# Kernel optimization log

Measured on AMD Instinct MI355X. Metric: run time of the kernel, lower is better.

The kernel has to match this reference:

```python
import jax, jax.numpy as jnp
import numpy as np

N, E, C_IN, H, K = 16384, 524288, 128, 64, 64


def setup_inputs() -> dict:
    key = jax.random.key(0)
    ks = jax.random.split(key, 6)
    x = jax.random.normal(ks[0], (N, C_IN), dtype=jnp.float32)
    edge_index = jax.random.randint(ks[1], (2, E), 0, N, dtype=jnp.int32)
    edge_weight = jax.random.uniform(ks[2], (E,), dtype=jnp.float32)
    sc = lambda f: 1.0 / np.sqrt(f)
    # GCNConv lin (no bias inside lin; separate bias), Glorot-ish init
    W1 = jax.random.normal(ks[3], (C_IN, H), dtype=jnp.float32) * sc(C_IN)
    b1 = jnp.zeros((H,), jnp.float32)
    # DMoNPooling MLP: Linear(H,H) then Linear(H,K), no activation between (act=None)
    Wm1 = jax.random.normal(ks[4], (H, H), dtype=jnp.float32) * sc(H)
    bm1 = jnp.zeros((H,), jnp.float32)
    Wm2 = jax.random.normal(ks[5], (H, K), dtype=jnp.float32) * sc(H)
    bm2 = jnp.zeros((K,), jnp.float32)
    return dict(x=x, edge_index=edge_index, edge_weight=edge_weight,
                W1=W1, b1=b1, Wm1=Wm1, bm1=bm1, Wm2=Wm2, bm2=bm2)


def gcn_conv(x, edge_index, edge_weight, W, b, n):
    # GCNConv: add self-loops (weight 1), symmetric deg^-1/2 normalization,
    # aggregate messages from source (row) into target (col).
    row, col = edge_index[0], edge_index[1]
    loop = jnp.arange(n, dtype=edge_index.dtype)
    row = jnp.concatenate([row, loop])
    col = jnp.concatenate([col, loop])
    w = jnp.concatenate([edge_weight, jnp.ones((n,), edge_weight.dtype)])
    deg = jax.ops.segment_sum(w, col, num_segments=n)
    dis = jnp.where(deg > 0, jax.lax.rsqrt(deg), 0.0)
    norm = dis[row] * w * dis[col]
    xw = x @ W  # [N, H]
    out = jax.ops.segment_sum(xw[row] * norm[:, None], col, num_segments=n)
    return out + b


def dmon_pool(h, adj, Wm1, bm1, Wm2, bm2):
    # eval mode: dropout disabled
    s = jax.nn.softmax((h @ Wm1 + bm1) @ Wm2 + bm2, axis=-1)  # [N, K]
    k = s.shape[-1]
    out_adj = s.T @ (adj @ s)  # [K, K]

    # Spectral (modularity) loss; degrees = einsum('ijk->ik', adj) = column sums
    deg = adj.sum(axis=0)  # [N]
    m = deg.sum() / 2
    ca = s.T @ deg  # [K], equals degrees^T s as well (symmetric roles)
    normalizer = jnp.outer(ca, ca) / 2 / m
    spectral_loss = -jnp.trace(out_adj - normalizer) / 2 / m

    # Orthogonality loss
    ss = s.T @ s  # [K, K]
    ss_fro = jnp.sqrt(jnp.sum(ss * ss))
    i_fro = jnp.sqrt(jnp.float32(k))  # ||I_K||_F
    diff = ss / ss_fro - jnp.eye(k, dtype=ss.dtype) / i_fro
    ortho_loss = jnp.sqrt(jnp.sum(diff * diff))

    # Cluster size loss
    cluster_size = s.sum(axis=0)  # [K]
    cluster_loss = jnp.sqrt(jnp.sum(cluster_size * cluster_size)) / h.shape[0] * i_fro - 1.0

    return s, spectral_loss, ortho_loss, cluster_loss


def reference(x, edge_index, edge_weight, W1, b1, Wm1, bm1, Wm2, bm2):
    h = jax.nn.relu(gcn_conv(x, edge_index, edge_weight, W1, b1, N))
    # to_dense_adj(edge_index): dense [N, N], duplicate edges summed
    adj = jnp.zeros((N, N), h.dtype).at[edge_index[0], edge_index[1]].add(1.0)
    s, spec, ortho, clus = dmon_pool(h, adj, Wm1, bm1, Wm2, bm2)
    return s[None], spec + ortho + clus
```

## Files before the change

### kernel.cpp

```cpp
#include <hip/hip_runtime.h>
#include <hip/hip_bf16.h>

typedef float          f4  __attribute__((ext_vector_type(4)));
typedef unsigned short us4 __attribute__((ext_vector_type(4)));
typedef int            i2  __attribute__((ext_vector_type(2)));

template <typename T>
__device__ __forceinline__ T ntload(const T* p) { return __builtin_nontemporal_load(p); }

__device__ __forceinline__ unsigned short f2bf(float f) {
    unsigned u = __float_as_uint(f);
    return (unsigned short)((u + 0x7FFF + ((u >> 16) & 1)) >> 16);
}
__device__ __forceinline__ float bf2f(unsigned short h) {
    return __uint_as_float((unsigned)h << 16);
}

__global__ __launch_bounds__(256) void k_degxw(const int* __restrict__ ei,
                      const float* __restrict__ ew,
                      unsigned long long* __restrict__ deg_rep,
                      const float* __restrict__ x, const float* __restrict__ W1,
                      float* __restrict__ xw, unsigned short* __restrict__ xw16,
                      int N, int E) {
    __shared__ float w1l[128 * 64];
    __shared__ f4    xt[16][32];
    if (blockIdx.x < 2048) {
        int e = blockIdx.x * 256 + threadIdx.x;
        if (e < E) {
            int c = ntload(ei + E + e);
            float w = ntload(ew + e);
            unsigned q = (unsigned)__float2uint_rn(w * 16777216.f);
            unsigned long long p = (1ULL << 40) | (unsigned long long)q;
            atomicAdd(&deg_rep[(size_t)(blockIdx.x & 7) * N + c], p);
        }
        return;
    }
    int xbid = blockIdx.x - 2048;
    for (int t = threadIdx.x; t < 128 * 64; t += 256) w1l[t] = W1[t];
    int lane = threadIdx.x & 63;
    int wv   = threadIdx.x >> 6;
    for (int base = xbid * 16; base < N; base += 512 * 16) {
        __syncthreads();
        for (int t = threadIdx.x; t < 16 * 32; t += 256)
            ((f4*)xt)[t] = ntload((const f4*)x + (size_t)base * 32 + t);
        __syncthreads();
        int r0 = wv * 4;
        float a0 = 0.f, a1 = 0.f, a2 = 0.f, a3 = 0.f;
#pragma unroll
        for (int q = 0; q < 32; ++q) {
            f4 x0 = xt[r0][q], x1 = xt[r0 + 1][q], x2 = xt[r0 + 2][q], x3 = xt[r0 + 3][q];
            float wa = w1l[(4 * q + 0) * 64 + lane];
            float wb = w1l[(4 * q + 1) * 64 + lane];
            float wc = w1l[(4 * q + 2) * 64 + lane];
            float wd = w1l[(4 * q + 3) * 64 + lane];
            a0 = fmaf(x0.x, wa, a0); a0 = fmaf(x0.y, wb, a0); a0 = fmaf(x0.z, wc, a0); a0 = fmaf(x0.w, wd, a0);
            a1 = fmaf(x1.x, wa, a1); a1 = fmaf(x1.y, wb, a1); a1 = fmaf(x1.z, wc, a1); a1 = fmaf(x1.w, wd, a1);
            a2 = fmaf(x2.x, wa, a2); a2 = fmaf(x2.y, wb, a2); a2 = fmaf(x2.z, wc, a2); a2 = fmaf(x2.w, wd, a2);
            a3 = fmaf(x3.x, wa, a3); a3 = fmaf(x3.y, wb, a3); a3 = fmaf(x3.z, wc, a3); a3 = fmaf(x3.w, wd, a3);
        }
        int gr = base + r0;
        __builtin_nontemporal_store(a0, xw + (size_t)(gr + 0) * 64 + lane);
        __builtin_nontemporal_store(a1, xw + (size_t)(gr + 1) * 64 + lane);
        __builtin_nontemporal_store(a2, xw + (size_t)(gr + 2) * 64 + lane);
        __builtin_nontemporal_store(a3, xw + (size_t)(gr + 3) * 64 + lane);
        xw16[(size_t)(gr + 0) * 64 + lane] = f2bf(a0);
        xw16[(size_t)(gr + 1) * 64 + lane] = f2bf(a1);
        xw16[(size_t)(gr + 2) * 64 + lane] = f2bf(a2);
        xw16[(size_t)(gr + 3) * 64 + lane] = f2bf(a3);
    }
}

__global__ void k_red(const unsigned long long* __restrict__ deg_rep,
                      int* __restrict__ off_rep, int* __restrict__ cnt,
                      float* __restrict__ dis, int N) {
    int c = blockIdx.x * blockDim.x + threadIdx.x;
    if (c >= N) return;
    int run = 0;
    unsigned long long wsum = 0;
#pragma unroll
    for (int rep = 0; rep < 8; ++rep) {
        unsigned long long p = deg_rep[(size_t)rep * N + c];
        off_rep[(size_t)rep * N + c] = run;
        run += (int)(p >> 40);
        wsum += (p & ((1ULL << 40) - 1));
    }
    cnt[c] = run;
    dis[c] = rsqrtf((float)wsum * (1.f / 16777216.f) + 1.0f);
}

__global__ void k_scan(const int* __restrict__ cnt, int* __restrict__ offs, int N) {
    __shared__ int part[1024];
    int tid = threadIdx.x;
    int C = (N + 1023) / 1024;
    int base = tid * C;
    int loc[16];
    int sum = 0;
#pragma unroll
    for (int i = 0; i < 16; ++i) {
        if (i < C) {
            int idx = base + i;
            loc[i] = sum;
            sum += (idx < N) ? cnt[idx] : 0;
        }
    }
    part[tid] = sum;
    __syncthreads();
    for (int o = 1; o < 1024; o <<= 1) {
        int t = (tid >= o) ? part[tid - o] : 0;
        __syncthreads();
        part[tid] += t;
        __syncthreads();
    }
    int excl = part[tid] - sum;
#pragma unroll
    for (int i = 0; i < 16; ++i) {
        if (i < C) {
            int idx = base + i;
            if (idx < N) offs[idx] = excl + loc[i];
        }
    }
    if (tid == 1023) offs[N] = part[tid];
}

__global__ void k_bucket(const int* __restrict__ ei, const float* __restrict__ ew,
                         const float* __restrict__ dis, const int* __restrict__ offs,
                         const int* __restrict__ off_rep, int* __restrict__ cursor_rep,
                         i2* __restrict__ barr, int N, int E) {
    int e = blockIdx.x * blockDim.x + threadIdx.x;
    if (e < E) {
        int rep = blockIdx.x & 7;
        int r = ntload(ei + e), c = ntload(ei + E + e);
        float norm = dis[r] * ntload(ew + e) * dis[c];
        size_t rc = (size_t)rep * N + c;
        int pos = offs[c] + off_rep[rc] + atomicAdd(&cursor_rep[rc], 1);
        i2 rec; rec.x = r; rec.y = __float_as_int(norm);
        __builtin_nontemporal_store(rec, barr + pos);
    }
}

__global__ __launch_bounds__(256) void k_gather(const int* __restrict__ offs,
                         const i2* __restrict__ barr,
                         const float* __restrict__ xw, const unsigned short* __restrict__ xw16,
                         const float* __restrict__ dis,
                         const float* __restrict__ b1, float* __restrict__ h, int N) {
    int lane = threadIdx.x & 63;
    int sub = lane >> 4, q = lane & 15;
    int wid  = blockIdx.x * 4 + (threadIdx.x >> 6);
    int nw   = 4 * gridDim.x;
    const us4* xw16v = (const us4*)xw16;
    for (int cp = wid; cp < (N >> 1); cp += nw) {
        int c0 = 2 * cp, c1 = c0 + 1;
        int beg = ntload(offs + c0), mid = ntload(offs + c1), end = ntload(offs + c1 + 1);
        f4 A0 = {0.f, 0.f, 0.f, 0.f}, A1 = A0, B0 = A0, B1 = A0;
        for (int i = beg; i < end; i += 64) {
            int nloc = min(64, end - i);
            bool ok = (i + lane < end);
            i2 b = ok ? ntload(barr + i + lane) : (i2){0, 0};
            int   rv = b.x;
            float nv = __int_as_float(b.y);
            int jmax = (nloc + 3) >> 2;
            int j = 0;
            for (; j + 4 <= jmax; j += 4) {
                int e0 = 4 * j + sub;
                int g0 = i + e0;
                int   r0 = __shfl(rv, e0),      r1 = __shfl(rv, e0 + 4);
                int   r2 = __shfl(rv, e0 + 8),  r3 = __shfl(rv, e0 + 12);
                float n0 = __shfl(nv, e0),      n1 = __shfl(nv, e0 + 4);
                float n2 = __shfl(nv, e0 + 8),  n3 = __shfl(nv, e0 + 12);
                us4 u0 = xw16v[(size_t)r0 * 16 + q];
                us4 u1 = xw16v[(size_t)r1 * 16 + q];
                us4 u2 = xw16v[(size_t)r2 * 16 + q];
                us4 u3 = xw16v[(size_t)r3 * 16 + q];
                float a0w = (g0      < mid) ? n0 : 0.f, b0w = n0 - a0w;
                float a1w = (g0 + 4  < mid) ? n1 : 0.f, b1w = n1 - a1w;
                float a2w = (g0 + 8  < mid) ? n2 : 0.f, b2w = n2 - a2w;
                float a3w = (g0 + 12 < mid) ? n3 : 0.f, b3w = n3 - a3w;
                A0.x = fmaf(bf2f(u0.x), a0w, A0.x); A0.y = fmaf(bf2f(u0.y), a0w, A0.y);
                A0.z = fmaf(bf2f(u0.z), a0w, A0.z); A0.w = fmaf(bf2f(u0.w), a0w, A0.w);
                B0.x = fmaf(bf2f(u0.x), b0w, B0.x); B0.y = fmaf(bf2f(u0.y), b0w, B0.y);
                B0.z = fmaf(bf2f(u0.z), b0w, B0.z); B0.w = fmaf(bf2f(u0.w), b0w, B0.w);
                A1.x = fmaf(bf2f(u1.x), a1w, A1.x); A1.y = fmaf(bf2f(u1.y), a1w, A1.y);
                A1.z = fmaf(bf2f(u1.z), a1w, A1.z); A1.w = fmaf(bf2f(u1.w), a1w, A1.w);
                B1.x = fmaf(bf2f(u1.x), b1w, B1.x); B1.y = fmaf(bf2f(u1.y), b1w, B1.y);
                B1.z = fmaf(bf2f(u1.z), b1w, B1.z); B1.w = fmaf(bf2f(u1.w), b1w, B1.w);
                A0.x = fmaf(bf2f(u2.x), a2w, A0.x); A0.y = fmaf(bf2f(u2.y), a2w, A0.y);
                A0.z = fmaf(bf2f(u2.z), a2w, A0.z); A0.w = fmaf(bf2f(u2.w), a2w, A0.w);
                B0.x = fmaf(bf2f(u2.x), b2w, B0.x); B0.y = fmaf(bf2f(u2.y), b2w, B0.y);
                B0.z = fmaf(bf2f(u2.z), b2w, B0.z); B0.w = fmaf(bf2f(u2.w), b2w, B0.w);
                A1.x = fmaf(bf2f(u3.x), a3w, A1.x); A1.y = fmaf(bf2f(u3.y), a3w, A1.y);
                A1.z = fmaf(bf2f(u3.z), a3w, A1.z); A1.w = fmaf(bf2f(u3.w), a3w, A1.w);
                B1.x = fmaf(bf2f(u3.x), b3w, B1.x); B1.y = fmaf(bf2f(u3.y), b3w, B1.y);
                B1.z = fmaf(bf2f(u3.z), b3w, B1.z); B1.w = fmaf(bf2f(u3.w), b3w, B1.w);
            }
            for (; j < jmax; ++j) {
                int e = 4 * j + sub;
                int g = i + e;
                int   r  = __shfl(rv, e);
                float nm = __shfl(nv, e);
                us4 u = xw16v[(size_t)r * 16 + q];
                float aw = (g < mid) ? nm : 0.f, bw = nm - aw;
                A0.x = fmaf(bf2f(u.x), aw, A0.x); A0.y = fmaf(bf2f(u.y), aw, A0.y);
                A0.z = fmaf(bf2f(u.z), aw, A0.z); A0.w = fmaf(bf2f(u.w), aw, A0.w);
                B0.x = fmaf(bf2f(u.x), bw, B0.x); B0.y = fmaf(bf2f(u.y), bw, B0.y);
                B0.z = fmaf(bf2f(u.z), bw, B0.z); B0.w = fmaf(bf2f(u.w), bw, B0.w);
            }
        }
        A0.x += A1.x; A0.y += A1.y; A0.z += A1.z; A0.w += A1.w;
        B0.x += B1.x; B0.y += B1.y; B0.z += B1.z; B0.w += B1.w;
        A0.x += __shfl_xor(A0.x, 16); A0.y += __shfl_xor(A0.y, 16);
        A0.z += __shfl_xor(A0.z, 16); A0.w += __shfl_xor(A0.w, 16);
        B0.x += __shfl_xor(B0.x, 16); B0.y += __shfl_xor(B0.y, 16);
        B0.z += __shfl_xor(B0.z, 16); B0.w += __shfl_xor(B0.w, 16);
        A0.x += __shfl_xor(A0.x, 32); A0.y += __shfl_xor(A0.y, 32);
        A0.z += __shfl_xor(A0.z, 32); A0.w += __shfl_xor(A0.w, 32);
        B0.x += __shfl_xor(B0.x, 32); B0.y += __shfl_xor(B0.y, 32);
        B0.z += __shfl_xor(B0.z, 32); B0.w += __shfl_xor(B0.w, 32);
        f4 bb = ((const f4*)b1)[q];
        f4 self0 = ntload((const f4*)xw + (size_t)c0 * 16 + q);
        f4 self1 = ntload((const f4*)xw + (size_t)c1 * 16 + q);
        float d0 = dis[c0], d1 = dis[c1];
        float dd0 = d0 * d0, dd1 = d1 * d1;
        f4 v0, v1;
        v0.x = A0.x + self0.x * dd0 + bb.x; v0.y = A0.y + self0.y * dd0 + bb.y;
        v0.z = A0.z + self0.z * dd0 + bb.z; v0.w = A0.w + self0.w * dd0 + bb.w;
        v1.x = B0.x + self1.x * dd1 + bb.x; v1.y = B0.y + self1.y * dd1 + bb.y;
        v1.z = B0.z + self1.z * dd1 + bb.z; v1.w = B0.w + self1.w * dd1 + bb.w;
        v0.x = v0.x > 0.f ? v0.x : 0.f; v0.y = v0.y > 0.f ? v0.y : 0.f;
        v0.z = v0.z > 0.f ? v0.z : 0.f; v0.w = v0.w > 0.f ? v0.w : 0.f;
        v1.x = v1.x > 0.f ? v1.x : 0.f; v1.y = v1.y > 0.f ? v1.y : 0.f;
        v1.z = v1.z > 0.f ? v1.z : 0.f; v1.w = v1.w > 0.f ? v1.w : 0.f;
        if (sub == 0) {
            __builtin_nontemporal_store(v0, (f4*)h + (size_t)c0 * 16 + q);
            __builtin_nontemporal_store(v1, (f4*)h + (size_t)c1 * 16 + q);
        }
    }
}

__global__ __launch_bounds__(256) void k_mlp(const float* __restrict__ h,
                      const float* __restrict__ Wm1, const float* __restrict__ bm1,
                      const float* __restrict__ Wm2, const float* __restrict__ bm2,
                      float* __restrict__ s, unsigned short* __restrict__ s16, int N) {
    __shared__ float w1l[4096], w2l[4096], b1l[64], b2l[64];
    __shared__ f4    ht[16][16];
    __shared__ float tt[4][4][64];
    for (int t = threadIdx.x; t < 4096; t += 256) {
        w1l[t] = Wm1[t];
        w2l[t] = Wm2[t];
    }
    if (threadIdx.x < 64) {
        b1l[threadIdx.x] = bm1[threadIdx.x];
        b2l[threadIdx.x] = bm2[threadIdx.x];
    }
    int lane = threadIdx.x & 63;
    int wv   = threadIdx.x >> 6;
    for (int base = blockIdx.x * 16; base < N; base += gridDim.x * 16) {
        __syncthreads();
        for (int t = threadIdx.x; t < 16 * 16; t += 256)
            ((f4*)ht)[t] = ntload((const f4*)h + (size_t)base * 16 + t);
        __syncthreads();
        int r0 = wv * 4;
        float t0 = b1l[lane], t1 = t0, t2 = t0, t3 = t0;
#pragma unroll
        for (int q = 0; q < 16; ++q) {
            f4 h0 = ht[r0][q], h1 = ht[r0 + 1][q], h2 = ht[r0 + 2][q], h3 = ht[r0 + 3][q];
            float wa = w1l[(4 * q + 0) * 64 + lane];
            float wb = w1l[(4 * q + 1) * 64 + lane];
            float wc = w1l[(4 * q + 2) * 64 + lane];
            float wd = w1l[(4 * q + 3) * 64 + lane];
            t0 = fmaf(h0.x, wa, t0); t0 = fmaf(h0.y, wb, t0); t0 = fmaf(h0.z, wc, t0); t0 = fmaf(h0.w, wd, t0);
            t1 = fmaf(h1.x, wa, t1); t1 = fmaf(h1.y, wb, t1); t1 = fmaf(h1.z, wc, t1); t1 = fmaf(h1.w, wd, t1);
            t2 = fmaf(h2.x, wa, t2); t2 = fmaf(h2.y, wb, t2); t2 = fmaf(h2.z, wc, t2); t2 = fmaf(h2.w, wd, t2);
            t3 = fmaf(h3.x, wa, t3); t3 = fmaf(h3.y, wb, t3); t3 = fmaf(h3.z, wc, t3); t3 = fmaf(h3.w, wd, t3);
        }
        tt[wv][0][lane] = t0; tt[wv][1][lane] = t1;
        tt[wv][2][lane] = t2; tt[wv][3][lane] = t3;
        __syncthreads();
        float g0 = b2l[lane], g1 = g0, g2 = g0, g3 = g0;
#pragma unroll
        for (int q = 0; q < 16; ++q) {
            f4 u0 = ((f4*)tt[wv][0])[q], u1 = ((f4*)tt[wv][1])[q];
            f4 u2 = ((f4*)tt[wv][2])[q], u3 = ((f4*)tt[wv][3])[q];
            float wa = w2l[(4 * q + 0) * 64 + lane];
            float wb = w2l[(4 * q + 1) * 64 + lane];
            float wc = w2l[(4 * q + 2) * 64 + lane];
            float wd = w2l[(4 * q + 3) * 64 + lane];
            g0 = fmaf(u0.x, wa, g0); g0 = fmaf(u0.y, wb, g0); g0 = fmaf(u0.z, wc, g0); g0 = fmaf(u0.w, wd, g0);
            g1 = fmaf(u1.x, wa, g1); g1 = fmaf(u1.y, wb, g1); g1 = fmaf(u1.z, wc, g1); g1 = fmaf(u1.w, wd, g1);
            g2 = fmaf(u2.x, wa, g2); g2 = fmaf(u2.y, wb, g2); g2 = fmaf(u2.z, wc, g2); g2 = fmaf(u2.w, wd, g2);
            g3 = fmaf(u3.x, wa, g3); g3 = fmaf(u3.y, wb, g3); g3 = fmaf(u3.z, wc, g3); g3 = fmaf(u3.w, wd, g3);
        }
        float m0 = g0, m1 = g1, m2 = g2, m3 = g3;
#pragma unroll
        for (int o = 32; o > 0; o >>= 1) {
            m0 = fmaxf(m0, __shfl_xor(m0, o));
            m1 = fmaxf(m1, __shfl_xor(m1, o));
            m2 = fmaxf(m2, __shfl_xor(m2, o));
            m3 = fmaxf(m3, __shfl_xor(m3, o));
        }
        float e0 = __expf(g0 - m0), e1 = __expf(g1 - m1);
        float e2 = __expf(g2 - m2), e3 = __expf(g3 - m3);
        float s0 = e0, s1 = e1, s2 = e2, s3 = e3;
#pragma unroll
        for (int o = 32; o > 0; o >>= 1) {
            s0 += __shfl_xor(s0, o);
            s1 += __shfl_xor(s1, o);
            s2 += __shfl_xor(s2, o);
            s3 += __shfl_xor(s3, o);
        }
        int gr = base + r0;
        float o0 = e0 / s0, o1 = e1 / s1, o2 = e2 / s2, o3 = e3 / s3;
        __builtin_nontemporal_store(o0, s + (size_t)(gr + 0) * 64 + lane);
        __builtin_nontemporal_store(o1, s + (size_t)(gr + 1) * 64 + lane);
        __builtin_nontemporal_store(o2, s + (size_t)(gr + 2) * 64 + lane);
        __builtin_nontemporal_store(o3, s + (size_t)(gr + 3) * 64 + lane);
        s16[(size_t)(gr + 0) * 64 + lane] = f2bf(o0);
        s16[(size_t)(gr + 1) * 64 + lane] = f2bf(o1);
        s16[(size_t)(gr + 2) * 64 + lane] = f2bf(o2);
        s16[(size_t)(gr + 3) * 64 + lane] = f2bf(o3);
    }
}

__global__ __launch_bounds__(256) void k_rt(const int* __restrict__ offs,
                         const i2* __restrict__ barr,
                         const unsigned short* __restrict__ s16,
                         const float* __restrict__ s, const int* __restrict__ cnt,
                         float* __restrict__ ssg, float* __restrict__ cag,
                         float* __restrict__ csg, float* __restrict__ tracearr, int N) {
    __shared__ float tile[64][64];
    __shared__ float bsum;
    int lane = threadIdx.x & 63;
    int wv   = threadIdx.x >> 6;
    if (blockIdx.x >= 2048) {
        int base = (blockIdx.x - 2048) * 64;
        if (base >= N) return;
        for (int t = threadIdx.x; t < 1024; t += 256)
            ((f4*)tile)[t] = ntload((const f4*)(s + (size_t)base * 64) + t);
        __syncthreads();
        float acc[16];
#pragma unroll
        for (int i = 0; i < 16; ++i) acc[i] = 0.f;
        for (int r = 0; r < 64; ++r) {
            float sj = tile[r][lane];
            const float* brow = &tile[r][wv * 16];
#pragma unroll
            for (int i = 0; i < 16; ++i) acc[i] = fmaf(brow[i], sj, acc[i]);
        }
        float csj = 0.f, caj = 0.f;
#pragma unroll
        for (int i = 0; i < 16; ++i) {
            int r = wv * 16 + i;
            float sj = tile[r][lane];
            csj += sj;
            caj = fmaf(sj, (float)cnt[base + r], caj);
        }
#pragma unroll
        for (int i = 0; i < 16; ++i) atomicAdd(&ssg[(wv * 16 + i) * 64 + lane], acc[i]);
        atomicAdd(&csg[lane], csj);
        atomicAdd(&cag[lane], caj);
        return;
    }
    int sub = lane >> 4, q = lane & 15;
    int wid  = blockIdx.x * 4 + wv;
    int nw   = 4 * 2048;
    const us4* s16v = (const us4*)s16;
    float tacc = 0.f;
    for (int cp = wid; cp < (N >> 1); cp += nw) {
        int c0 = 2 * cp, c1 = c0 + 1;
        int beg = ntload(offs + c0), mid = ntload(offs + c1), end = ntload(offs + c1 + 1);
        us4 scu0 = s16v[(size_t)c0 * 16 + q];
        us4 scu1 = s16v[(size_t)c1 * 16 + q];
        f4 sc0 = {bf2f(scu0.x), bf2f(scu0.y), bf2f(scu0.z), bf2f(scu0.w)};
        f4 sc1 = {bf2f(scu1.x), bf2f(scu1.y), bf2f(scu1.z), bf2f(scu1.w)};
        f4 A0 = {0.f, 0.f, 0.f, 0.f}, A1 = A0, B0 = A0, B1 = A0;
        for (int i = beg; i < end; i += 64) {
            int nloc = min(64, end - i);
            int rv = (i + lane < end) ? ntload(barr + i + lane).x : 0;
            int jmax = (nloc + 3) >> 2;
            int j = 0;
            for (; j + 4 <= jmax; j += 4) {
                int e0 = 4 * j + sub;
                int g0 = i + e0;
                int r0 = __shfl(rv, e0),     r1 = __shfl(rv, e0 + 4);
                int r2 = __shfl(rv, e0 + 8), r3 = __shfl(rv, e0 + 12);
                float n0 = (e0      < nloc) ? 1.f : 0.f;
                float n1 = (e0 + 4  < nloc) ? 1.f : 0.f;
                float n2 = (e0 + 8  < nloc) ? 1.f : 0.f;
                float n3 = (e0 + 12 < nloc) ? 1.f : 0.f;
                us4 u0 = s16v[(size_t)r0 * 16 + q];
                us4 u1 = s16v[(size_t)r1 * 16 + q];
                us4 u2 = s16v[(size_t)r2 * 16 + q];
                us4 u3 = s16v[(size_t)r3 * 16 + q];
                float a0w = (g0      < mid) ? n0 : 0.f, b0w = n0 - a0w;
                float a1w = (g0 + 4  < mid) ? n1 : 0.f, b1w = n1 - a1w;
                float a2w = (g0 + 8  < mid) ? n2 : 0.f, b2w = n2 - a2w;
                float a3w = (g0 + 12 < mid) ? n3 : 0.f, b3w = n3 - a3w;
                A0.x = fmaf(bf2f(u0.x), a0w, A0.x); A0.y = fmaf(bf2f(u0.y), a0w, A0.y);
                A0.z = fmaf(bf2f(u0.z), a0w, A0.z); A0.w = fmaf(bf2f(u0.w), a0w, A0.w);
                B0.x = fmaf(bf2f(u0.x), b0w, B0.x); B0.y = fmaf(bf2f(u0.y), b0w, B0.y);
                B0.z = fmaf(bf2f(u0.z), b0w, B0.z); B0.w = fmaf(bf2f(u0.w), b0w, B0.w);
                A1.x = fmaf(bf2f(u1.x), a1w, A1.x); A1.y = fmaf(bf2f(u1.y), a1w, A1.y);
                A1.z = fmaf(bf2f(u1.z), a1w, A1.z); A1.w = fmaf(bf2f(u1.w), a1w, A1.w);
                B1.x = fmaf(bf2f(u1.x), b1w, B1.x); B1.y = fmaf(bf2f(u1.y), b1w, B1.y);
                B1.z = fmaf(bf2f(u1.z), b1w, B1.z); B1.w = fmaf(bf2f(u1.w), b1w, B1.w);
                A0.x = fmaf(bf2f(u2.x), a2w, A0.x); A0.y = fmaf(bf2f(u2.y), a2w, A0.y);
                A0.z = fmaf(bf2f(u2.z), a2w, A0.z); A0.w = fmaf(bf2f(u2.w), a2w, A0.w);
                B0.x = fmaf(bf2f(u2.x), b2w, B0.x); B0.y = fmaf(bf2f(u2.y), b2w, B0.y);
                B0.z = fmaf(bf2f(u2.z), b2w, B0.z); B0.w = fmaf(bf2f(u2.w), b2w, B0.w);
                A1.x = fmaf(bf2f(u3.x), a3w, A1.x); A1.y = fmaf(bf2f(u3.y), a3w, A1.y);
                A1.z = fmaf(bf2f(u3.z), a3w, A1.z); A1.w = fmaf(bf2f(u3.w), a3w, A1.w);
                B1.x = fmaf(bf2f(u3.x), b3w, B1.x); B1.y = fmaf(bf2f(u3.y), b3w, B1.y);
                B1.z = fmaf(bf2f(u3.z), b3w, B1.z); B1.w = fmaf(bf2f(u3.w), b3w, B1.w);
            }
            for (; j < jmax; ++j) {
                int e = 4 * j + sub;
                int g = i + e;
                int r = __shfl(rv, e);
                float m = (e < nloc) ? 1.f : 0.f;
                us4 u = s16v[(size_t)r * 16 + q];
                float aw = (g < mid) ? m : 0.f, bw = m - aw;
                A0.x = fmaf(bf2f(u.x), aw, A0.x); A0.y = fmaf(bf2f(u.y), aw, A0.y);
                A0.z = fmaf(bf2f(u.z), aw, A0.z); A0.w = fmaf(bf2f(u.w), aw, A0.w);
                B0.x = fmaf(bf2f(u.x), bw, B0.x); B0.y = fmaf(bf2f(u.y), bw, B0.y);
                B0.z = fmaf(bf2f(u.z), bw, B0.z); B0.w = fmaf(bf2f(u.w), bw, B0.w);
            }
        }
        A0.x += A1.x; A0.y += A1.y; A0.z += A1.z; A0.w += A1.w;
        B0.x += B1.x; B0.y += B1.y; B0.z += B1.z; B0.w += B1.w;
        A0.x += __shfl_xor(A0.x, 16); A0.y += __shfl_xor(A0.y, 16);
        A0.z += __shfl_xor(A0.z, 16); A0.w += __shfl_xor(A0.w, 16);
        B0.x += __shfl_xor(B0.x, 16); B0.y += __shfl_xor(B0.y, 16);
        B0.z += __shfl_xor(B0.z, 16); B0.w += __shfl_xor(B0.w, 16);
        A0.x += __shfl_xor(A0.x, 32); A0.y += __shfl_xor(A0.y, 32);
        A0.z += __shfl_xor(A0.z, 32); A0.w += __shfl_xor(A0.w, 32);
        B0.x += __shfl_xor(B0.x, 32); B0.y += __shfl_xor(B0.y, 32);
        B0.z += __shfl_xor(B0.z, 32); B0.w += __shfl_xor(B0.w, 32);
        tacc += A0.x * sc0.x + A0.y * sc0.y + A0.z * sc0.z + A0.w * sc0.w;
        tacc += B0.x * sc1.x + B0.y * sc1.y + B0.z * sc1.z + B0.w * sc1.w;
    }
    tacc *= 0.25f;
#pragma unroll
    for (int o = 32; o > 0; o >>= 1) tacc += __shfl_xor(tacc, o);
    if (threadIdx.x == 0) bsum = 0.f;
    __syncthreads();
    if (lane == 0) atomicAdd(&bsum, tacc);
    __syncthreads();
    if (threadIdx.x == 0) tracearr[blockIdx.x] = bsum;
}

__global__ void k_final(const float* __restrict__ ssg, const float* __restrict__ cag,
                        const float* __restrict__ csg, const float* __restrict__ tracearr,
                        int ntr, float Ef, float Nf, float* __restrict__ out) {
    __shared__ float red[256];
    int tid = threadIdx.x;

    float a = 0.f;
    for (int t = tid; t < ntr; t += 256) a += tracearr[t];
    red[tid] = a; __syncthreads();
    for (int o = 128; o > 0; o >>= 1) { if (tid < o) red[tid] += red[tid + o]; __syncthreads(); }
    float trace = red[0]; __syncthreads();

    a = 0.f;
    for (int t = tid; t < 4096; t += 256) { float v = ssg[t]; a += v * v; }
    red[tid] = a; __syncthreads();
    for (int o = 128; o > 0; o >>= 1) { if (tid < o) red[tid] += red[tid + o]; __syncthreads(); }
    float ss_sumsq = red[0]; __syncthreads();

    a = (tid < 64) ? ssg[tid * 64 + tid] : 0.f;
    red[tid] = a; __syncthreads();
    for (int o = 128; o > 0; o >>= 1) { if (tid < o) red[tid] += red[tid + o]; __syncthreads(); }
    float tr_ss = red[0]; __syncthreads();

    a = (tid < 64) ? cag[tid] * cag[tid] : 0.f;
    red[tid] = a; __syncthreads();
    for (int o = 128; o > 0; o >>= 1) { if (tid < o) red[tid] += red[tid + o]; __syncthreads(); }
    float ca_ss = red[0]; __syncthreads();

    a = (tid < 64) ? csg[tid] * csg[tid] : 0.f;
    red[tid] = a; __syncthreads();
    for (int o = 128; o > 0; o >>= 1) { if (tid < o) red[tid] += red[tid + o]; __syncthreads(); }
    float cs_ss = red[0];

    if (tid == 0) {
        float spec = -(trace - ca_ss / Ef) / Ef;
        float ss_fro = sqrtf(ss_sumsq);
        float ortho = sqrtf(fmaxf(2.f - tr_ss / (4.f * ss_fro), 0.f));
        float clus = sqrtf(cs_ss) / Nf * 8.f - 1.f;
        out[0] = spec + ortho + clus;
    }
}

extern "C" void kernel_launch(void* const* d_in, const int* in_sizes, int n_in,
                              void* d_out, int out_size, void* d_ws, size_t ws_size,
                              hipStream_t stream) {
    const float* x   = (const float*)d_in[0];
    const int*   ei  = (const int*)d_in[1];
    const float* ew  = (const float*)d_in[2];
    const float* W1  = (const float*)d_in[3];
    const float* b1  = (const float*)d_in[4];
    const float* Wm1 = (const float*)d_in[5];
    const float* bm1 = (const float*)d_in[6];
    const float* Wm2 = (const float*)d_in[7];
    const float* bm2 = (const float*)d_in[8];
    float* out = (float*)d_out;

    const int N = in_sizes[0] / 128;
    const int E = in_sizes[2];
    const int TGRID = 2304;

    char* base = (char*)d_ws;
    unsigned long long* deg_rep = (unsigned long long*)base;
    int*   cursor_rep = (int*)(base + (size_t)64 * N);
    float* ssg = (float*)(base + (size_t)96 * N);
    float* cag = ssg + 4096;
    float* csg = cag + 64;
    size_t zbytes = (size_t)96 * N + (4096 + 128) * 4;
    char* up = base + ((zbytes + 15) & ~(size_t)15);
    int*   cnt = (int*)up;            up += (size_t)4 * N;
    float* dis = (float*)up;          up += (size_t)4 * N;
    int*   offs = (int*)up;           up += (size_t)4 * (N + 1);
    float* tracearr = (float*)up;     up += (size_t)4 * TGRID;
    up = (char*)(((size_t)up + 15) & ~(size_t)15);
    float* xw = (float*)up;           up += (size_t)4 * N * 64;
    float* h  = (float*)up;           up += (size_t)4 * N * 64;
    int*   off_rep = (int*)h;
    i2*    barr = (i2*)up;            up += (size_t)8 * E;
    unsigned short* xw16 = (unsigned short*)up; up += (size_t)2 * N * 64;
    unsigned short* s16  = (unsigned short*)up;
    float* sbuf = out;

    hipMemsetAsync(d_ws, 0, zbytes, stream);

    k_degxw<<<2560, 256, 0, stream>>>(ei, ew, deg_rep, x, W1, xw, xw16, N, E);
    k_red<<<(N + 255) / 256, 256, 0, stream>>>(deg_rep, off_rep, cnt, dis, N);
    k_scan<<<1, 1024, 0, stream>>>(cnt, offs, N);
    k_bucket<<<(E + 255) / 256, 256, 0, stream>>>(ei, ew, dis, offs, off_rep, cursor_rep, barr, N, E);
    k_gather<<<2048, 256, 0, stream>>>(offs, barr, xw, xw16, dis, b1, h, N);
    k_mlp<<<512, 256, 0, stream>>>(h, Wm1, bm1, Wm2, bm2, sbuf, s16, N);
    k_rt<<<TGRID, 256, 0, stream>>>(offs, barr, s16, sbuf, cnt, ssg, cag, csg, tracearr, N);
    k_final<<<1, 256, 0, stream>>>(ssg, cag, csg, tracearr, TGRID, (float)E, (float)N,
                                   out + (size_t)N * 64);
}
```

Measured before the change: 234.6 us.

## Fuse the MLP and softmax into the gather kernel and drop the fp32 xw buffer

The separate MLP kernel is merged into the gather kernel. Each wave now computes the two-layer MLP and softmax for its pair of aggregated rows, using shuffles to broadcast h and bf16 weights staged in LDS. This removes the round trip of h through global memory, one kernel launch, and the fp32 xw write and read; the self-loop term now uses the bf16 copy. The cost is extra shuffle and LDS traffic per row pair, duplicated weight staging in each of the 2048 blocks, and reduced precision from bf16 weights and self terms.

```diff
diff --git a/kernel.cpp b/kernel.cpp
--- a/kernel.cpp
+++ b/kernel.cpp
@@ -20,7 +20,7 @@
                       const float* __restrict__ ew,
                       unsigned long long* __restrict__ deg_rep,
                       const float* __restrict__ x, const float* __restrict__ W1,
-                      float* __restrict__ xw, unsigned short* __restrict__ xw16,
+                      unsigned short* __restrict__ xw16,
                       int N, int E) {
     __shared__ float w1l[128 * 64];
     __shared__ f4    xt[16][32];
@@ -59,10 +59,6 @@
             a3 = fmaf(x3.x, wa, a3); a3 = fmaf(x3.y, wb, a3); a3 = fmaf(x3.z, wc, a3); a3 = fmaf(x3.w, wd, a3);
         }
         int gr = base + r0;
-        __builtin_nontemporal_store(a0, xw + (size_t)(gr + 0) * 64 + lane);
-        __builtin_nontemporal_store(a1, xw + (size_t)(gr + 1) * 64 + lane);
-        __builtin_nontemporal_store(a2, xw + (size_t)(gr + 2) * 64 + lane);
-        __builtin_nontemporal_store(a3, xw + (size_t)(gr + 3) * 64 + lane);
         xw16[(size_t)(gr + 0) * 64 + lane] = f2bf(a0);
         xw16[(size_t)(gr + 1) * 64 + lane] = f2bf(a1);
         xw16[(size_t)(gr + 2) * 64 + lane] = f2bf(a2);
@@ -138,11 +134,24 @@
     }
 }
 
-__global__ __launch_bounds__(256) void k_gather(const int* __restrict__ offs,
+__global__ __launch_bounds__(256) void k_gathmlp(const int* __restrict__ offs,
                          const i2* __restrict__ barr,
-                         const float* __restrict__ xw, const unsigned short* __restrict__ xw16,
-                         const float* __restrict__ dis,
-                         const float* __restrict__ b1, float* __restrict__ h, int N) {
+                         const unsigned short* __restrict__ xw16,
+                         const float* __restrict__ dis, const float* __restrict__ b1,
+                         const float* __restrict__ Wm1, const float* __restrict__ bm1,
+                         const float* __restrict__ Wm2, const float* __restrict__ bm2,
+                         float* __restrict__ s, unsigned short* __restrict__ s16, int N) {
+    __shared__ unsigned short w1l[4096], w2l[4096];
+    __shared__ float b1m[64], b2m[64];
+    for (int t = threadIdx.x; t < 4096; t += 256) {
+        w1l[t] = f2bf(Wm1[t]);
+        w2l[t] = f2bf(Wm2[t]);
+    }
+    if (threadIdx.x < 64) {
+        b1m[threadIdx.x] = bm1[threadIdx.x];
+        b2m[threadIdx.x] = bm2[threadIdx.x];
+    }
+    __syncthreads();
     int lane = threadIdx.x & 63;
     int sub = lane >> 4, q = lane & 15;
     int wid  = blockIdx.x * 4 + (threadIdx.x >> 6);
@@ -216,107 +225,69 @@
         B0.x += __shfl_xor(B0.x, 32); B0.y += __shfl_xor(B0.y, 32);
         B0.z += __shfl_xor(B0.z, 32); B0.w += __shfl_xor(B0.w, 32);
         f4 bb = ((const f4*)b1)[q];
-        f4 self0 = ntload((const f4*)xw + (size_t)c0 * 16 + q);
-        f4 self1 = ntload((const f4*)xw + (size_t)c1 * 16 + q);
+        us4 su0 = xw16v[(size_t)c0 * 16 + q];
+        us4 su1 = xw16v[(size_t)c1 * 16 + q];
         float d0 = dis[c0], d1 = dis[c1];
         float dd0 = d0 * d0, dd1 = d1 * d1;
         f4 v0, v1;
-        v0.x = A0.x + self0.x * dd0 + bb.x; v0.y = A0.y + self0.y * dd0 + bb.y;
-        v0.z = A0.z + self0.z * dd0 + bb.z; v0.w = A0.w + self0.w * dd0 + bb.w;
-        v1.x = B0.x + self1.x * dd1 + bb.x; v1.y = B0.y + self1.y * dd1 + bb.y;
-        v1.z = B0.z + self1.z * dd1 + bb.z; v1.w = B0.w + self1.w * dd1 + bb.w;
+        v0.x = A0.x + bf2f(su0.x) * dd0 + bb.x; v0.y = A0.y + bf2f(su0.y) * dd0 + bb.y;
+        v0.z = A0.z + bf2f(su0.z) * dd0 + bb.z; v0.w = A0.w + bf2f(su0.w) * dd0 + bb.w;
+        v1.x = B0.x + bf2f(su1.x) * dd1 + bb.x; v1.y = B0.y + bf2f(su1.y) * dd1 + bb.y;
+        v1.z = B0.z + bf2f(su1.z) * dd1 + bb.z; v1.w = B0.w + bf2f(su1.w) * dd1 + bb.w;
         v0.x = v0.x > 0.f ? v0.x : 0.f; v0.y = v0.y > 0.f ? v0.y : 0.f;
         v0.z = v0.z > 0.f ? v0.z : 0.f; v0.w = v0.w > 0.f ? v0.w : 0.f;
         v1.x = v1.x > 0.f ? v1.x : 0.f; v1.y = v1.y > 0.f ? v1.y : 0.f;
         v1.z = v1.z > 0.f ? v1.z : 0.f; v1.w = v1.w > 0.f ? v1.w : 0.f;
-        if (sub == 0) {
-            __builtin_nontemporal_store(v0, (f4*)h + (size_t)c0 * 16 + q);
-            __builtin_nontemporal_store(v1, (f4*)h + (size_t)c1 * 16 + q);
-        }
-    }
-}
-
-__global__ __launch_bounds__(256) void k_mlp(const float* __restrict__ h,
-                      const float* __restrict__ Wm1, const float* __restrict__ bm1,
-                      const float* __restrict__ Wm2, const float* __restrict__ bm2,
-                      float* __restrict__ s, unsigned short* __restrict__ s16, int N) {
-    __shared__ float w1l[4096], w2l[4096], b1l[64], b2l[64];
-    __shared__ f4    ht[16][16];
-    __shared__ float tt[4][4][64];
-    for (int t = threadIdx.x; t < 4096; t += 256) {
-        w1l[t] = Wm1[t];
-        w2l[t] = Wm2[t];
-    }
-    if (threadIdx.x < 64) {
-        b1l[threadIdx.x] = bm1[threadIdx.x];
-        b2l[threadIdx.x] = bm2[threadIdx.x];
-    }
-    int lane = threadIdx.x & 63;
-    int wv   = threadIdx.x >> 6;
-    for (int base = blockIdx.x * 16; base < N; base += gridDim.x * 16) {
-        __syncthreads();
-        for (int t = threadIdx.x; t < 16 * 16; t += 256)
-            ((f4*)ht)[t] = ntload((const f4*)h + (size_t)base * 16 + t);
-        __syncthreads();
-        int r0 = wv * 4;
-        float t0 = b1l[lane], t1 = t0, t2 = t0, t3 = t0;
-#pragma unroll
-        for (int q = 0; q < 16; ++q) {
-            f4 h0 = ht[r0][q], h1 = ht[r0 + 1][q], h2 = ht[r0 + 2][q], h3 = ht[r0 + 3][q];
-            float wa = w1l[(4 * q + 0) * 64 + lane];
-            float wb = w1l[(4 * q + 1) * 64 + lane];
-            float wc = w1l[(4 * q + 2) * 64 + lane];
-            float wd = w1l[(4 * q + 3) * 64 + lane];
-            t0 = fmaf(h0.x, wa, t0); t0 = fmaf(h0.y, wb, t0); t0 = fmaf(h0.z, wc, t0); t0 = fmaf(h0.w, wd, t0);
-            t1 = fmaf(h1.x, wa, t1); t1 = fmaf(h1.y, wb, t1); t1 = fmaf(h1.z, wc, t1); t1 = fmaf(h1.w, wd, t1);
-            t2 = fmaf(h2.x, wa, t2); t2 = fmaf(h2.y, wb, t2); t2 = fmaf(h2.z, wc, t2); t2 = fmaf(h2.w, wd, t2);
-            t3 = fmaf(h3.x, wa, t3); t3 = fmaf(h3.y, wb, t3); t3 = fmaf(h3.z, wc, t3); t3 = fmaf(h3.w, wd, t3);
-        }
-        tt[wv][0][lane] = t0; tt[wv][1][lane] = t1;
-        tt[wv][2][lane] = t2; tt[wv][3][lane] = t3;
-        __syncthreads();
-        float g0 = b2l[lane], g1 = g0, g2 = g0, g3 = g0;
-#pragma unroll
-        for (int q = 0; q < 16; ++q) {
-            f4 u0 = ((f4*)tt[wv][0])[q], u1 = ((f4*)tt[wv][1])[q];
-            f4 u2 = ((f4*)tt[wv][2])[q], u3 = ((f4*)tt[wv][3])[q];
-            float wa = w2l[(4 * q + 0) * 64 + lane];
-            float wb = w2l[(4 * q + 1) * 64 + lane];
-            float wc = w2l[(4 * q + 2) * 64 + lane];
-            float wd = w2l[(4 * q + 3) * 64 + lane];
-            g0 = fmaf(u0.x, wa, g0); g0 = fmaf(u0.y, wb, g0); g0 = fmaf(u0.z, wc, g0); g0 = fmaf(u0.w, wd, g0);
-            g1 = fmaf(u1.x, wa, g1); g1 = fmaf(u1.y, wb, g1); g1 = fmaf(u1.z, wc, g1); g1 = fmaf(u1.w, wd, g1);
-            g2 = fmaf(u2.x, wa, g2); g2 = fmaf(u2.y, wb, g2); g2 = fmaf(u2.z, wc, g2); g2 = fmaf(u2.w, wd, g2);
-            g3 = fmaf(u3.x, wa, g3); g3 = fmaf(u3.y, wb, g3); g3 = fmaf(u3.z, wc, g3); g3 = fmaf(u3.w, wd, g3);
-        }
-        float m0 = g0, m1 = g1, m2 = g2, m3 = g3;
+        float tA = b1m[lane], tB = tA;
+#pragma unroll
+        for (int k4 = 0; k4 < 16; ++k4) {
+            float h00 = __shfl(v0.x, k4), h01 = __shfl(v0.y, k4);
+            float h02 = __shfl(v0.z, k4), h03 = __shfl(v0.w, k4);
+            float h10 = __shfl(v1.x, k4), h11 = __shfl(v1.y, k4);
+            float h12 = __shfl(v1.z, k4), h13 = __shfl(v1.w, k4);
+            float wa = bf2f(w1l[(4 * k4 + 0) * 64 + lane]);
+            float wb = bf2f(w1l[(4 * k4 + 1) * 64 + lane]);
+            float wc = bf2f(w1l[(4 * k4 + 2) * 64 + lane]);
+            float wd = bf2f(w1l[(4 * k4 + 3) * 64 + lane]);
+            tA = fmaf(h00, wa, tA); tA = fmaf(h01, wb, tA);
+            tA = fmaf(h02, wc, tA); tA = fmaf(h03, wd, tA);
+            tB = fmaf(h10, wa, tB); tB = fmaf(h11, wb, tB);
+            tB = fmaf(h12, wc, tB); tB = fmaf(h13, wd, tB);
+        }
+        float gA = b2m[lane], gB = gA;
+#pragma unroll
+        for (int k4 = 0; k4 < 16; ++k4) {
+            float tA0 = __shfl(tA, 4 * k4),     tA1 = __shfl(tA, 4 * k4 + 1);
+            float tA2 = __shfl(tA, 4 * k4 + 2), tA3 = __shfl(tA, 4 * k4 + 3);
+            float tB0 = __shfl(tB, 4 * k4),     tB1 = __shfl(tB, 4 * k4 + 1);
+            float tB2 = __shfl(tB, 4 * k4 + 2), tB3 = __shfl(tB, 4 * k4 + 3);
+            float wa = bf2f(w2l[(4 * k4 + 0) * 64 + lane]);
+            float wb = bf2f(w2l[(4 * k4 + 1) * 64 + lane]);
+            float wc = bf2f(w2l[(4 * k4 + 2) * 64 + lane]);
+            float wd = bf2f(w2l[(4 * k4 + 3) * 64 + lane]);
+            gA = fmaf(tA0, wa, gA); gA = fmaf(tA1, wb, gA);
+            gA = fmaf(tA2, wc, gA); gA = fmaf(tA3, wd, gA);
+            gB = fmaf(tB0, wa, gB); gB = fmaf(tB1, wb, gB);
+            gB = fmaf(tB2, wc, gB); gB = fmaf(tB3, wd, gB);
+        }
+        float mA = gA, mB = gB;
 #pragma unroll
         for (int o = 32; o > 0; o >>= 1) {
-            m0 = fmaxf(m0, __shfl_xor(m0, o));
-            m1 = fmaxf(m1, __shfl_xor(m1, o));
-            m2 = fmaxf(m2, __shfl_xor(m2, o));
-            m3 = fmaxf(m3, __shfl_xor(m3, o));
-        }
-        float e0 = __expf(g0 - m0), e1 = __expf(g1 - m1);
-        float e2 = __expf(g2 - m2), e3 = __expf(g3 - m3);
-        float s0 = e0, s1 = e1, s2 = e2, s3 = e3;
+            mA = fmaxf(mA, __shfl_xor(mA, o));
+            mB = fmaxf(mB, __shfl_xor(mB, o));
+        }
+        float eA = __expf(gA - mA), eB = __expf(gB - mB);
+        float sA = eA, sB = eB;
 #pragma unroll
         for (int o = 32; o > 0; o >>= 1) {
-            s0 += __shfl_xor(s0, o);
-            s1 += __shfl_xor(s1, o);
-            s2 += __shfl_xor(s2, o);
-            s3 += __shfl_xor(s3, o);
-        }
-        int gr = base + r0;
-        float o0 = e0 / s0, o1 = e1 / s1, o2 = e2 / s2, o3 = e3 / s3;
-        __builtin_nontemporal_store(o0, s + (size_t)(gr + 0) * 64 + lane);
-        __builtin_nontemporal_store(o1, s + (size_t)(gr + 1) * 64 + lane);
-        __builtin_nontemporal_store(o2, s + (size_t)(gr + 2) * 64 + lane);
-        __builtin_nontemporal_store(o3, s + (size_t)(gr + 3) * 64 + lane);
-        s16[(size_t)(gr + 0) * 64 + lane] = f2bf(o0);
-        s16[(size_t)(gr + 1) * 64 + lane] = f2bf(o1);
-        s16[(size_t)(gr + 2) * 64 + lane] = f2bf(o2);
-        s16[(size_t)(gr + 3) * 64 + lane] = f2bf(o3);
+            sA += __shfl_xor(sA, o);
+            sB += __shfl_xor(sB, o);
+        }
+        float oA = eA / sA, oB = eB / sB;
+        __builtin_nontemporal_store(oA, s + (size_t)c0 * 64 + lane);
+        __builtin_nontemporal_store(oB, s + (size_t)c1 * 64 + lane);
+        s16[(size_t)c0 * 64 + lane] = f2bf(oA);
+        s16[(size_t)c1 * 64 + lane] = f2bf(oB);
     }
 }
 
@@ -520,9 +491,7 @@
     int*   offs = (int*)up;           up += (size_t)4 * (N + 1);
     float* tracearr = (float*)up;     up += (size_t)4 * TGRID;
     up = (char*)(((size_t)up + 15) & ~(size_t)15);
-    float* xw = (float*)up;           up += (size_t)4 * N * 64;
-    float* h  = (float*)up;           up += (size_t)4 * N * 64;
-    int*   off_rep = (int*)h;
+    int*   off_rep = (int*)up;        up += (size_t)32 * N;
     i2*    barr = (i2*)up;            up += (size_t)8 * E;
     unsigned short* xw16 = (unsigned short*)up; up += (size_t)2 * N * 64;
     unsigned short* s16  = (unsigned short*)up;
@@ -530,12 +499,12 @@
 
     hipMemsetAsync(d_ws, 0, zbytes, stream);
 
-    k_degxw<<<2560, 256, 0, stream>>>(ei, ew, deg_rep, x, W1, xw, xw16, N, E);
+    k_degxw<<<2560, 256, 0, stream>>>(ei, ew, deg_rep, x, W1, xw16, N, E);
     k_red<<<(N + 255) / 256, 256, 0, stream>>>(deg_rep, off_rep, cnt, dis, N);
     k_scan<<<1, 1024, 0, stream>>>(cnt, offs, N);
     k_bucket<<<(E + 255) / 256, 256, 0, stream>>>(ei, ew, dis, offs, off_rep, cursor_rep, barr, N, E);
-    k_gather<<<2048, 256, 0, stream>>>(offs, barr, xw, xw16, dis, b1, h, N);
-    k_mlp<<<512, 256, 0, stream>>>(h, Wm1, bm1, Wm2, bm2, sbuf, s16, N);
+    k_gathmlp<<<2048, 256, 0, stream>>>(offs, barr, xw16, dis, b1, Wm1, bm1, Wm2, bm2,
+                                        sbuf, s16, N);
     k_rt<<<TGRID, 256, 0, stream>>>(offs, barr, s16, sbuf, cnt, ssg, cag, csg, tracearr, N);
     k_final<<<1, 256, 0, stream>>>(ssg, cag, csg, tracearr, TGRID, (float)E, (float)N,
                                    out + (size_t)N * 64);
```

Measured after the change: 280.6 us. 19.6% more time.
